# Performance work log

Measured on AMD Instinct MI355X. Metric: run time of the kernel, lower is better.

## Reference

```python
import jax, jax.numpy as jnp
import numpy as np

EPS = 1e-5


def _extract3x3(x, stride=1):
    # channel-major patch extraction: output [B, C*9, Ho, Wo], each channel's 3x3 window contiguous
    B, C, H, W = x.shape
    xp = jnp.pad(x, ((0, 0), (0, 0), (1, 1), (1, 1)))
    Ho = (H + 2 - 3) // stride + 1
    Wo = (W + 2 - 3) // stride + 1
    pats = [xp[:, :, i:i + (Ho - 1) * stride + 1:stride, j:j + (Wo - 1) * stride + 1:stride]
            for i in range(3) for j in range(3)]
    return jnp.stack(pats, axis=2).reshape(B, C * 9, Ho, Wo)


def _amm(patches, centroids, lut, inv_temp):
    # patches: [B, D, H, W] channel-major, D = ncodebooks * subvec_len
    # centroids: [ncb, k, sub], lut: [ncb, k, out_channels]
    B, D, H, W = patches.shape
    ncb, k, sub = centroids.shape
    v = patches.reshape(B, ncb, sub, H * W).transpose(0, 3, 1, 2)  # [B, L, ncb, sub]
    # negative squared distance to each codeword (||v||^2 dropped: constant over k)
    scores = 2.0 * jnp.einsum('blcs,cks->blck', v, centroids) - jnp.sum(centroids * centroids, -1)[None, None]
    attn = jax.nn.softmax(scores * inv_temp, axis=-1)          # soft codeword assignment
    out = jnp.einsum('blck,cko->blo', attn, lut)                # LUT gather/sum over codebooks
    return out.transpose(0, 2, 1).reshape(B, -1, H, W)


def _bn(x, g, b):
    m = x.mean((0, 2, 3), keepdims=True)
    v = x.var((0, 2, 3), keepdims=True)
    return g[None, :, None, None] * (x - m) * jax.lax.rsqrt(v + EPS) + b[None, :, None, None]


def setup_inputs() -> dict:
    key = jax.random.key(0)
    ks = jax.random.split(key, 8)
    B, C, H, W = 32, 1024, 14, 14
    width, out_c, K = 256, 1024, 16
    return {
        'x': jax.random.normal(ks[0], (B, C, H, W), jnp.float32),
        'c1_centroids': jax.random.normal(ks[1], (C // 4, K, 4), jnp.float32),
        'c1_lut': jax.random.normal(ks[2], (C // 4, K, width), jnp.float32) * 0.05,
        'c1_invt': jnp.ones((), jnp.float32),
        'c2_centroids': jax.random.normal(ks[3], (width, K, 9), jnp.float32),
        'c2_lut': jax.random.normal(ks[4], (width, K, width), jnp.float32) * 0.05,
        'c2_invt': jnp.ones((), jnp.float32),
        'c3_centroids': jax.random.normal(ks[5], (width // 4, K, 4), jnp.float32),
        'c3_lut': jax.random.normal(ks[6], (width // 4, K, out_c), jnp.float32) * 0.05,
        'c3_invt': jnp.ones((), jnp.float32),
        'bn1_g': jnp.ones((width,), jnp.float32), 'bn1_b': jnp.zeros((width,), jnp.float32),
        'bn2_g': jnp.ones((width,), jnp.float32), 'bn2_b': jnp.zeros((width,), jnp.float32),
        'bn3_g': jnp.ones((out_c,), jnp.float32), 'bn3_b': jnp.zeros((out_c,), jnp.float32),
    }


def reference(x, c1_centroids, c1_lut, c1_invt, c2_centroids, c2_lut, c2_invt,
              c3_centroids, c3_lut, c3_invt, bn1_g, bn1_b, bn2_g, bn2_b, bn3_g, bn3_b):
    identity = x
    out = _amm(x, c1_centroids, c1_lut, c1_invt)                 # amm_conv1x1, stride 1
    out = jax.nn.relu(_bn(out, bn1_g, bn1_b))
    out = _amm(_extract3x3(out, 1), c2_centroids, c2_lut, c2_invt)  # amm_conv3x3, stride 1, pad 1
    out = jax.nn.relu(_bn(out, bn2_g, bn2_b))
    out = _amm(out, c3_centroids, c3_lut, c3_invt)               # amm_conv1x1
    out = _bn(out, bn3_g, bn3_b)
    return jax.nn.relu(out + identity)
```

## Files before the change

kernel.cpp:

```cpp
#include <hip/hip_runtime.h>
#include <hip/hip_bf16.h>

#define EPSV 1e-5f

typedef unsigned short u16;
typedef __attribute__((ext_vector_type(8))) short short8;
typedef __attribute__((ext_vector_type(4))) float f32x4;
typedef __hip_bfloat16 bf16;

__device__ __forceinline__ unsigned int pack2(float a, float b) {
  bf16 ha = __float2bfloat16(a), hb = __float2bfloat16(b);
  u16 ua, ub;
  __builtin_memcpy(&ua, &ha, 2);
  __builtin_memcpy(&ub, &hb, 2);
  return (unsigned int)ua | ((unsigned int)ub << 16);
}

typedef __attribute__((address_space(1))) const void gvoid_t;
typedef __attribute__((address_space(3))) void lvoid_t;
__device__ __forceinline__ void gload16(const void* g, void* l) {
  __builtin_amdgcn_global_load_lds((gvoid_t*)g, (lvoid_t*)l, 16, 0, 0);
}


__global__ __launch_bounds__(256) void prep_kernel(
    const float* __restrict__ x, const float* __restrict__ cent,
    const float* __restrict__ invt, u16* __restrict__ attn,
    const float* __restrict__ s1, bf16* __restrict__ d1,
    const float* __restrict__ s2, bf16* __restrict__ d2,
    const float* __restrict__ s3, bf16* __restrict__ d3)
{
  __shared__ __align__(16) float sh[4160];
  const int tid = threadIdx.x;
  if (blockIdx.x >= 3584) {
    const int bid = blockIdx.x - 3584;
    const int which = bid >> 8, sub = bid & 255;
    const float* in = (which == 0) ? s1 : (which == 1) ? s2 : s3;
    bf16* out = (which == 0) ? d1 : (which == 1) ? d2 : d3;
    const int K = (which == 2) ? 1024 : 4096;
    const int N = (which == 2) ? 1024 : 256;
    const int kt = K >> 6;
    const int bk = sub & (kt - 1), bn = sub / kt;
    const int k0 = bk * 64, n0 = bn * 64;
    float* t = sh;
    for (int idx = tid; idx < 4096; idx += 256) {
      int r = idx >> 6, c = idx & 63;
      t[r * 65 + c] = in[(size_t)(k0 + r) * N + n0 + c];
    }
    __syncthreads();
    for (int idx = tid; idx < 4096; idx += 256) {
      int r = idx >> 6, c = idx & 63;
      out[(size_t)(n0 + r) * K + k0 + c] = __float2bfloat16(t[c * 65 + r]);
    }
    return;
  }
  float* vs = sh;
  float* cs = sh + 1848;
  const int row = blockIdx.x >> 3, cg = blockIdx.x & 7;
  const int m0 = row * 14;
  const int b = row / 14, y = row - b * 14;
  const float* xb = x + ((size_t)b * 1024 + cg * 128) * 196 + y * 14;
  for (int e = tid; e < 1792; e += 256) {
    int c = e / 14, p = e - c * 14;
    vs[p * 132 + c] = xb[(size_t)c * 196 + p];
  }
  for (int idx = tid; idx < 512; idx += 256) {
    int cb = idx >> 4, kk = idx & 15;
    *(float4*)&cs[cb * 68 + kk * 4] =
        *(const float4*)&cent[(size_t)(cg * 32 + cb) * 64 + kk * 4];
  }
  __syncthreads();
  const float it = invt[0];
  const int cb = tid & 31, pq = tid >> 5;
  const int np = (pq < 6) ? 2 : 1;
  float4 v[2];
  v[0] = *(const float4*)&vs[pq * 132 + cb * 4];
  if (np > 1) v[1] = *(const float4*)&vs[(8 + pq) * 132 + cb * 4];
  float s[2][16];
  #pragma unroll
  for (int k = 0; k < 16; k++) {
    const float4 c = *(const float4*)&cs[cb * 68 + k * 4];
    const float cn = c.x * c.x + c.y * c.y + c.z * c.z + c.w * c.w;
    #pragma unroll
    for (int i = 0; i < 2; i++) if (i < np) {
      float d = v[i].x * c.x + v[i].y * c.y + v[i].z * c.z + v[i].w * c.w;
      s[i][k] = it * (2.f * d - cn);
    }
  }
  #pragma unroll
  for (int i = 0; i < 2; i++) if (i < np) {
    float mx = -3e38f;
    #pragma unroll
    for (int k = 0; k < 16; k++) mx = fmaxf(mx, s[i][k]);
    float sum = 0.f;
    #pragma unroll
    for (int k = 0; k < 16; k++) { float e = __expf(s[i][k] - mx); s[i][k] = e; sum += e; }
    const float r = 1.f / sum;
    uint4 w0, w1;
    w0.x = pack2(s[i][0] * r,  s[i][1] * r);  w0.y = pack2(s[i][2] * r,  s[i][3] * r);
    w0.z = pack2(s[i][4] * r,  s[i][5] * r);  w0.w = pack2(s[i][6] * r,  s[i][7] * r);
    w1.x = pack2(s[i][8] * r,  s[i][9] * r);  w1.y = pack2(s[i][10] * r, s[i][11] * r);
    w1.z = pack2(s[i][12] * r, s[i][13] * r); w1.w = pack2(s[i][14] * r, s[i][15] * r);
    uint4* dst = (uint4*)(attn + (size_t)(m0 + i * 8 + pq) * 4096 + (cg * 32 + cb) * 16);
    dst[0] = w0; dst[1] = w1;
  }
}

__global__ __launch_bounds__(256) void attn2_kernel(const float* __restrict__ out1,
    const float* __restrict__ ss, const float* __restrict__ cent,
    const float* __restrict__ invt, u16* __restrict__ attn)
{
  __shared__ float vs[4 * 16 * 32];
  __shared__ __align__(16) float cs[32 * 196];
  const int tid = threadIdx.x;
  const int rp = blockIdx.x >> 3, cg = blockIdx.x & 7;
  const int b = rp / 7, y0 = (rp % 7) * 2, m0 = rp * 28;
  for (int e = tid; e < 2048; e += 256) {
    int c = e & 31, x1 = (e >> 5) & 15, dyy = e >> 9;
    int yy = y0 + dyy - 1, xx = x1 - 1;
    float v = 0.f;
    int ch = cg * 32 + c;
    if (yy >= 0 && yy < 14 && xx >= 0 && xx < 14) {
      float val = out1[(size_t)((b * 14 + yy) * 14 + xx) * 256 + ch];
      v = fmaxf(val * ss[ch] + ss[256 + ch], 0.f);
    }
    vs[e] = v;
  }
  for (int idx = tid; idx < 1152; idx += 256) {
    int cb = idx / 36, f4i = idx - cb * 36;
    float4 w = *(const float4*)&cent[(size_t)(cg * 32 + cb) * 144 + f4i * 4];
    int j0 = f4i * 4;
    #pragma unroll
    for (int t = 0; t < 4; t++) {
      int j = j0 + t, k = j / 9, jj = j - k * 9;
      cs[cb * 196 + k * 12 + jj] = ((const float*)&w)[t];
    }
  }
  __syncthreads();
  const float it = invt[0];
  const int cb = tid & 31, pq = tid >> 5;
  const int np = (pq < 4) ? 4 : 3;
  float v[4][9];
  #pragma unroll
  for (int i = 0; i < 4; i++) if (i < np) {
    const int p = i * 8 + pq;
    const int r = p / 14, xc = p - r * 14;
    #pragma unroll
    for (int dy = 0; dy < 3; dy++)
      #pragma unroll
      for (int dx = 0; dx < 3; dx++)
        v[i][dy * 3 + dx] = vs[((r + dy) * 16 + xc + dx) * 32 + cb];
  }
  float s[4][16];
  #pragma unroll
  for (int k = 0; k < 16; k++) {
    const float* ck = &cs[cb * 196 + k * 12];
    const float4 ca = *(const float4*)ck;
    const float4 cbv = *(const float4*)(ck + 4);
    const float c8 = ck[8];
    float c9[9] = {ca.x, ca.y, ca.z, ca.w, cbv.x, cbv.y, cbv.z, cbv.w, c8};
    float cn = 0.f;
    #pragma unroll
    for (int j = 0; j < 9; j++) cn = fmaf(c9[j], c9[j], cn);
    #pragma unroll
    for (int i = 0; i < 4; i++) if (i < np) {
      float d = 0.f;
      #pragma unroll
      for (int j = 0; j < 9; j++) d = fmaf(c9[j], v[i][j], d);
      s[i][k] = it * (2.f * d - cn);
    }
  }
  #pragma unroll
  for (int i = 0; i < 4; i++) if (i < np) {
    float mx = -3e38f;
    #pragma unroll
    for (int k = 0; k < 16; k++) mx = fmaxf(mx, s[i][k]);
    float sum = 0.f;
    #pragma unroll
    for (int k = 0; k < 16; k++) { float e = __expf(s[i][k] - mx); s[i][k] = e; sum += e; }
    const float r = 1.f / sum;
    uint4 w0, w1;
    w0.x = pack2(s[i][0] * r,  s[i][1] * r);  w0.y = pack2(s[i][2] * r,  s[i][3] * r);
    w0.z = pack2(s[i][4] * r,  s[i][5] * r);  w0.w = pack2(s[i][6] * r,  s[i][7] * r);
    w1.x = pack2(s[i][8] * r,  s[i][9] * r);  w1.y = pack2(s[i][10] * r, s[i][11] * r);
    w1.z = pack2(s[i][12] * r, s[i][13] * r); w1.w = pack2(s[i][14] * r, s[i][15] * r);
    uint4* dst = (uint4*)(attn + (size_t)(m0 + i * 8 + pq) * 4096 + (cg * 32 + cb) * 16);
    dst[0] = w0; dst[1] = w1;
  }
}

__global__ __launch_bounds__(256) void attn3_kernel(const float* __restrict__ out2,
    const float* __restrict__ ss, const float* __restrict__ cent,
    const float* __restrict__ invt, bf16* __restrict__ attn)
{
  const int t = threadIdx.x;
  const int cb = t & 63, ml = t >> 6;
  const int m0 = blockIdx.x * 16;
  const float it = invt[0];
  float4 cv[16]; float cn[16];
  const float4* cc = (const float4*)(cent + cb * 64);
  #pragma unroll
  for (int k = 0; k < 16; k++) {
    cv[k] = cc[k];
    cn[k] = cv[k].x * cv[k].x + cv[k].y * cv[k].y + cv[k].z * cv[k].z + cv[k].w * cv[k].w;
  }
  const float4 scv = *(const float4*)(ss + cb * 4);
  const float4 shv = *(const float4*)(ss + 256 + cb * 4);
  for (int g = 0; g < 4; g++) {
    const int m = m0 + g * 4 + ml;
    float4 xv = *(const float4*)(out2 + (size_t)m * 256 + cb * 4);
    float4 v;
    v.x = fmaxf(xv.x * scv.x + shv.x, 0.f);
    v.y = fmaxf(xv.y * scv.y + shv.y, 0.f);
    v.z = fmaxf(xv.z * scv.z + shv.z, 0.f);
    v.w = fmaxf(xv.w * scv.w + shv.w, 0.f);
    float s[16], mx = -3e38f;
    #pragma unroll
    for (int k = 0; k < 16; k++) {
      float d = v.x * cv[k].x + v.y * cv[k].y + v.z * cv[k].z + v.w * cv[k].w;
      s[k] = it * (2.f * d - cn[k]);
      mx = fmaxf(mx, s[k]);
    }
    float sum = 0.f;
    #pragma unroll
    for (int k = 0; k < 16; k++) { float e = __expf(s[k] - mx); s[k] = e; sum += e; }
    float r = 1.f / sum;
    #pragma unroll
    for (int k = 0; k < 16; k++)
      attn[(size_t)m * 1024 + cb * 16 + k] = __float2bfloat16(s[k] * r);
  }
}

template<int KDIM, int NT, int KSLICES, int BM, int BK>
__global__ __launch_bounds__(256) void gemm_kernel(const u16* __restrict__ A,
    const u16* __restrict__ Bt, float* __restrict__ C, size_t cstride)
{
  constexpr int NDIM = NT * 128;
  constexpr int KS = KDIM / KSLICES;
  constexpr int MT = 6272 / BM;
  constexpr int FM = BM / 32;
  constexpr int KU = BK / 32;
  constexpr int SLOTS = BK / 8;
  constexpr int RPC = 64 / SLOTS;
  constexpr int ACALLS = BM / (RPC * 4);
  constexpr int BCALLS = 128 / (RPC * 4);
  __shared__ __align__(16) u16 Asm[BM * BK];
  __shared__ __align__(16) u16 Bsm[128 * BK];
  const int tid = threadIdx.x;
  const int nt = blockIdx.x % NT;
  const int mt = (blockIdx.x / NT) % MT;
  const int sl = blockIdx.x / (NT * MT);
  const int kbeg = sl * KS, kend = kbeg + KS;
  const int m0 = mt * BM, n0 = nt * 128;
  const int lane = tid & 63, wid = tid >> 6;
  const int wm = wid >> 1, wn = wid & 1;
  const int lr = lane / SLOTS, sslot = lane % SLOTS;

  f32x4 acc[FM][4];
  #pragma unroll
  for (int i = 0; i < FM; i++)
    #pragma unroll
    for (int j = 0; j < 4; j++) acc[i][j] = (f32x4){0.f, 0.f, 0.f, 0.f};

  const u16* Abase = A + (size_t)m0 * KDIM;
  const u16* Bbase = Bt + (size_t)n0 * KDIM;

  for (int kb = kbeg; kb < kend; kb += BK) {
    #pragma unroll
    for (int c = 0; c < ACALLS; c++) {
      const int r0 = (wid * ACALLS + c) * RPC;
      const int row = r0 + lr;
      const int gs = sslot ^ (row & 7);
      gload16(Abase + (size_t)row * KDIM + kb + gs * 8, &Asm[r0 * BK]);
    }
    #pragma unroll
    for (int c = 0; c < BCALLS; c++) {
      const int r0 = (wid * BCALLS + c) * RPC;
      const int row = r0 + lr;
      const int gs = sslot ^ (row & 7);
      gload16(Bbase + (size_t)row * KDIM + kb + gs * 8, &Bsm[r0 * BK]);
    }
    __syncthreads();
    #pragma unroll
    for (int ks = 0; ks < KU; ks++) {
      short8 a[FM], b[4];
      #pragma unroll
      for (int f = 0; f < FM; f++) {
        const int ra = wm * (BM / 2) + f * 16 + (lane & 15);
        const int ja = (ks * 4 + (lane >> 4)) ^ (ra & 7);
        a[f] = *(const short8*)(Asm + ra * BK + ja * 8);
      }
      #pragma unroll
      for (int f = 0; f < 4; f++) {
        const int rb = wn * 64 + f * 16 + (lane & 15);
        const int jb = (ks * 4 + (lane >> 4)) ^ (rb & 7);
        b[f] = *(const short8*)(Bsm + rb * BK + jb * 8);
      }
      #pragma unroll
      for (int fm = 0; fm < FM; fm++)
        #pragma unroll
        for (int fn = 0; fn < 4; fn++)
          acc[fm][fn] = __builtin_amdgcn_mfma_f32_16x16x32_bf16(a[fm], b[fn], acc[fm][fn], 0, 0, 0);
    }
    __syncthreads();
  }

  float* __restrict__ Cs = C + (size_t)sl * cstride;
  #pragma unroll
  for (int fm = 0; fm < FM; fm++)
    #pragma unroll
    for (int fn = 0; fn < 4; fn++) {
      const int col = n0 + wn * 64 + fn * 16 + (lane & 15);
      const int rbase = m0 + wm * (BM / 2) + fm * 16 + (lane >> 4) * 4;
      #pragma unroll
      for (int r = 0; r < 4; r++)
        Cs[(size_t)(rbase + r) * NDIM + col] = acc[fm][fn][r];
    }
}

template<int CH, int NBLK, int NSUM>
__global__ __launch_bounds__(256) void bnpart_kernel(const float* __restrict__ buf,
    float* __restrict__ sum_out, float* __restrict__ part)
{
  constexpr int PC = CH / 256;
  constexpr int ROWS = 6272 / NBLK;
  constexpr size_t PSTR = 6272ull * CH;
  const int t = threadIdx.x, m0 = blockIdx.x * ROWS;
  float s[PC], s2[PC];
  #pragma unroll
  for (int j = 0; j < PC; j++) { s[j] = 0.f; s2[j] = 0.f; }
  for (int i = 0; i < ROWS; i++) {
    const size_t ro = (size_t)(m0 + i) * CH;
    #pragma unroll
    for (int j = 0; j < PC; j++) {
      float v = buf[ro + t + j * 256];
      #pragma unroll
      for (int n = 1; n < NSUM; n++) v += buf[(size_t)n * PSTR + ro + t + j * 256];
      if (NSUM > 1) sum_out[ro + t + j * 256] = v;
      s[j] += v; s2[j] = fmaf(v, v, s2[j]);
    }
  }
  #pragma unroll
  for (int j = 0; j < PC; j++) {
    part[(size_t)blockIdx.x * (2 * CH) + t + j * 256] = s[j];
    part[(size_t)blockIdx.x * (2 * CH) + CH + t + j * 256] = s2[j];
  }
}

template<int CH, int NBLK>
__global__ __launch_bounds__(256) void bnfin_kernel(const float* __restrict__ part,
    const float* __restrict__ g, const float* __restrict__ bb, float* __restrict__ ss)
{
  __shared__ float red[2][4][64];
  const int t = threadIdx.x;
  const int chl = t & 63, grp = t >> 6;
  const int c = blockIdx.x * 64 + chl;
  float S = 0.f, S2 = 0.f;
  for (int i = grp; i < NBLK; i += 4) {
    S += part[(size_t)i * (2 * CH) + c];
    S2 += part[(size_t)i * (2 * CH) + CH + c];
  }
  red[0][grp][chl] = S; red[1][grp][chl] = S2;
  __syncthreads();
  if (t < 64) {
    float Sf  = red[0][0][t] + red[0][1][t] + red[0][2][t] + red[0][3][t];
    float S2f = red[1][0][t] + red[1][1][t] + red[1][2][t] + red[1][3][t];
    const int ch = blockIdx.x * 64 + t;
    float mean = Sf * (1.f / 6272.f);
    float var = S2f * (1.f / 6272.f) - mean * mean;
    float sc = g[ch] * rsqrtf(var + EPSV);
    ss[ch] = sc;
    ss[CH + ch] = bb[ch] - mean * sc;
  }
}

__global__ __launch_bounds__(256) void tfinal_kernel(const float* __restrict__ out3,
    const float* __restrict__ ss, const float* __restrict__ x, float* __restrict__ out)
{
  __shared__ float t[64 * 199];
  const int b = blockIdx.x >> 4, n0 = (blockIdx.x & 15) * 64;
  for (int idx = threadIdx.x; idx < 196 * 64; idx += 256) {
    int p = idx >> 6, ni = idx & 63;
    float v = out3[(size_t)(b * 196 + p) * 1024 + n0 + ni] * ss[n0 + ni] + ss[1024 + n0 + ni];
    t[ni * 199 + p] = v;
  }
  __syncthreads();
  for (int idx = threadIdx.x; idx < 64 * 196; idx += 256) {
    int ni = idx / 196, p = idx - ni * 196;
    size_t o = (size_t)(b * 1024 + n0 + ni) * 196 + p;
    out[o] = fmaxf(t[ni * 199 + p] + x[o], 0.f);
  }
}


template<int CIN, int OUT, bool APPLY_BN>
__global__ __launch_bounds__(256) void amm1x1_kernel(
    const float* __restrict__ xin, const float* __restrict__ ss,
    const float* __restrict__ cent, const float* __restrict__ lut,
    const float* __restrict__ invt, float* __restrict__ outbuf)
{
  constexpr int NCB = CIN / 4;
  constexpr int NO = OUT / 256;
  __shared__ float vsm[CIN * 14];
  __shared__ __align__(16) float attn_sm[14 * 16];
  const int tid = threadIdx.x;
  const int b = blockIdx.x / 14, y = blockIdx.x % 14;
  const int rowbase = y * 14;
  for (int e = tid; e < CIN * 14; e += 256) {
    int c = e / 14, xc = e - c * 14;
    float v = xin[(b * CIN + c) * 196 + rowbase + xc];
    if (APPLY_BN) v = fmaxf(v * ss[c] + ss[CIN + c], 0.f);
    vsm[e] = v;
  }
  __syncthreads();
  float acc[14 * NO];
  #pragma unroll
  for (int i = 0; i < 14 * NO; i++) acc[i] = 0.f;
  const float it = invt[0];
  const int p_ = tid >> 4, k_ = tid & 15;
  for (int cb = 0; cb < NCB; ++cb) {
    if (tid < 224) {
      const float* cc = cent + (cb * 16 + k_) * 4;
      float s = 0.f;
      #pragma unroll
      for (int si = 0; si < 4; si++) {
        float cv = cc[si];
        float vv = vsm[(cb * 4 + si) * 14 + p_];
        s = fmaf(cv, 2.f * vv - cv, s);
      }
      s *= it;
      float m = s;
      #pragma unroll
      for (int off = 8; off; off >>= 1) m = fmaxf(m, __shfl_xor(m, off, 16));
      float e = __expf(s - m);
      float sum = e;
      #pragma unroll
      for (int off = 8; off; off >>= 1) sum += __shfl_xor(sum, off, 16);
      attn_sm[p_ * 16 + k_] = e / sum;
    }
    __syncthreads();
    float lv[NO][16];
    #pragma unroll
    for (int j = 0; j < NO; j++)
      #pragma unroll
      for (int k = 0; k < 16; k++)
        lv[j][k] = lut[(cb * 16 + k) * OUT + j * 256 + tid];
    const float4* a4 = (const float4*)attn_sm;
    #pragma unroll
    for (int p = 0; p < 14; p++) {
      float4 q0 = a4[p*4+0], q1 = a4[p*4+1], q2 = a4[p*4+2], q3 = a4[p*4+3];
      float av[16] = {q0.x,q0.y,q0.z,q0.w, q1.x,q1.y,q1.z,q1.w,
                      q2.x,q2.y,q2.z,q2.w, q3.x,q3.y,q3.z,q3.w};
      #pragma unroll
      for (int j = 0; j < NO; j++) {
        float s = acc[p * NO + j];
        #pragma unroll
        for (int k = 0; k < 16; k++) s = fmaf(av[k], lv[j][k], s);
        acc[p * NO + j] = s;
      }
    }
    __syncthreads();
  }
  #pragma unroll
  for (int j = 0; j < NO; j++) {
    int o = j * 256 + tid;
    #pragma unroll
    for (int p = 0; p < 14; p++)
      outbuf[(b * OUT + o) * 196 + rowbase + p] = acc[p * NO + j];
  }
}

__global__ __launch_bounds__(256) void amm3x3_kernel(
    const float* __restrict__ xin, const float* __restrict__ ss,
    const float* __restrict__ cent, const float* __restrict__ lut,
    const float* __restrict__ invt, float* __restrict__ outbuf)
{
  __shared__ float vsm[256 * 3 * 16];
  __shared__ __align__(16) float attn_sm[14 * 16];
  const int tid = threadIdx.x;
  const int b = blockIdx.x / 14, y = blockIdx.x % 14;
  for (int e = tid; e < 256 * 3 * 16; e += 256) {
    int c = e / 48, rem = e - c * 48, i = rem >> 4, col = rem & 15;
    int yy = y + i - 1, xx = col - 1;
    float v = 0.f;
    if (yy >= 0 && yy < 14 && xx >= 0 && xx < 14) {
      v = xin[(b * 256 + c) * 196 + yy * 14 + xx];
      v = fmaxf(v * ss[c] + ss[256 + c], 0.f);
    }
    vsm[e] = v;
  }
  __syncthreads();
  float acc[14];
  #pragma unroll
  for (int i = 0; i < 14; i++) acc[i] = 0.f;
  const float it = invt[0];
  const int p_ = tid >> 4, k_ = tid & 15;
  for (int cb = 0; cb < 256; ++cb) {
    if (tid < 224) {
      const float* cc = cent + (cb * 16 + k_) * 9;
      float s = 0.f;
      #pragma unroll
      for (int i = 0; i < 3; i++)
        #pragma unroll
        for (int j = 0; j < 3; j++) {
          float cv = cc[i * 3 + j];
          float vv = vsm[(cb * 3 + i) * 16 + p_ + j];
          s = fmaf(cv, 2.f * vv - cv, s);
        }
      s *= it;
      float m = s;
      #pragma unroll
      for (int off = 8; off; off >>= 1) m = fmaxf(m, __shfl_xor(m, off, 16));
      float e = __expf(s - m);
      float sum = e;
      #pragma unroll
      for (int off = 8; off; off >>= 1) sum += __shfl_xor(sum, off, 16);
      attn_sm[p_ * 16 + k_] = e / sum;
    }
    __syncthreads();
    float lv[16];
    #pragma unroll
    for (int k = 0; k < 16; k++) lv[k] = lut[(cb * 16 + k) * 256 + tid];
    const float4* a4 = (const float4*)attn_sm;
    #pragma unroll
    for (int p = 0; p < 14; p++) {
      float4 q0 = a4[p*4+0], q1 = a4[p*4+1], q2 = a4[p*4+2], q3 = a4[p*4+3];
      float av[16] = {q0.x,q0.y,q0.z,q0.w, q1.x,q1.y,q1.z,q1.w,
                      q2.x,q2.y,q2.z,q2.w, q3.x,q3.y,q3.z,q3.w};
      float s = acc[p];
      #pragma unroll
      for (int k = 0; k < 16; k++) s = fmaf(av[k], lv[k], s);
      acc[p] = s;
    }
    __syncthreads();
  }
  #pragma unroll
  for (int p = 0; p < 14; p++)
    outbuf[(b * 256 + tid) * 196 + y * 14 + p] = acc[p];
}

template<int CH>
__global__ __launch_bounds__(256) void bnstats_kernel(const float* __restrict__ buf,
    const float* __restrict__ g, const float* __restrict__ bb, float* __restrict__ ss)
{
  const int c = blockIdx.x, tid = threadIdx.x;
  float s = 0.f, s2 = 0.f;
  for (int e = tid; e < 32 * 196; e += 256) {
    int bi = e / 196, l = e - bi * 196;
    float v = buf[(bi * CH + c) * 196 + l];
    s += v; s2 = fmaf(v, v, s2);
  }
  #pragma unroll
  for (int off = 32; off; off >>= 1) { s += __shfl_down(s, off); s2 += __shfl_down(s2, off); }
  __shared__ float red[8];
  int w = tid >> 6;
  if ((tid & 63) == 0) { red[w] = s; red[4 + w] = s2; }
  __syncthreads();
  if (tid == 0) {
    float S  = red[0] + red[1] + red[2] + red[3];
    float S2 = red[4] + red[5] + red[6] + red[7];
    float mean = S * (1.f / 6272.f);
    float var  = S2 * (1.f / 6272.f) - mean * mean;
    float sc = g[c] * rsqrtf(var + EPSV);
    ss[c] = sc;
    ss[CH + c] = bb[c] - mean * sc;
  }
}

__global__ __launch_bounds__(256) void final_old_kernel(float* __restrict__ out3,
    const float* __restrict__ ss, const float* __restrict__ x)
{
  const int total = 32 * 1024 * 196;
  for (int idx = blockIdx.x * 256 + threadIdx.x; idx < total; idx += gridDim.x * 256) {
    int c = (idx / 196) & 1023;
    float v = out3[idx] * ss[c] + ss[1024 + c] + x[idx];
    out3[idx] = fmaxf(v, 0.f);
  }
}


extern "C" void kernel_launch(void* const* d_in, const int* in_sizes, int n_in,
                              void* d_out, int out_size, void* d_ws, size_t ws_size,
                              hipStream_t stream) {
  const float* x   = (const float*)d_in[0];
  const float* c1c = (const float*)d_in[1];
  const float* c1l = (const float*)d_in[2];
  const float* c1t = (const float*)d_in[3];
  const float* c2c = (const float*)d_in[4];
  const float* c2l = (const float*)d_in[5];
  const float* c2t = (const float*)d_in[6];
  const float* c3c = (const float*)d_in[7];
  const float* c3l = (const float*)d_in[8];
  const float* c3t = (const float*)d_in[9];
  const float* g1  = (const float*)d_in[10];
  const float* b1  = (const float*)d_in[11];
  const float* g2  = (const float*)d_in[12];
  const float* b2  = (const float*)d_in[13];
  const float* g3  = (const float*)d_in[14];
  const float* b3  = (const float*)d_in[15];

  float* ws = (float*)d_ws;
  const size_t FAST_NEED = 24255488ull * 4ull;

  if (ws_size >= FAST_NEED) {
    u16*   attnB = (u16*)ws;
    float* partC = ws + 12845056;
    float* out1  = partC + 6422528;
    float* out2  = out1 + 1605632;
    bf16*  lutT1 = (bf16*)(out2 + 1605632);
    bf16*  lutT2 = lutT1 + 1048576;
    bf16*  lutT3 = lutT2 + 1048576;
    float* part  = (float*)(lutT3 + 1048576);
    float* ss1   = part + 200704;
    float* ss2   = ss1 + 512;
    float* ss3   = ss2 + 512;
    float* out3  = partC;
    const size_t PART_STRIDE = 1605632;

    prep_kernel<<<4352, 256, 0, stream>>>(x, c1c, c1t, attnB,
                                          c1l, lutT1, c2l, lutT2, c3l, lutT3);

    gemm_kernel<4096, 2, 4, 128, 128><<<392, 256, 0, stream>>>(attnB, (const u16*)lutT1, partC, PART_STRIDE);
    bnpart_kernel<256, 196, 4><<<196, 256, 0, stream>>>(partC, out1, part);
    bnfin_kernel<256, 196><<<4, 256, 0, stream>>>(part, g1, b1, ss1);

    attn2_kernel<<<1792, 256, 0, stream>>>(out1, ss1, c2c, c2t, attnB);
    gemm_kernel<4096, 2, 4, 128, 128><<<392, 256, 0, stream>>>(attnB, (const u16*)lutT2, partC, PART_STRIDE);
    bnpart_kernel<256, 196, 4><<<196, 256, 0, stream>>>(partC, out2, part);
    bnfin_kernel<256, 196><<<4, 256, 0, stream>>>(part, g2, b2, ss2);

    attn3_kernel<<<392, 256, 0, stream>>>(out2, ss2, c3c, c3t, (bf16*)attnB);
    gemm_kernel<1024, 8, 1, 128, 128><<<392, 256, 0, stream>>>(attnB, (const u16*)lutT3, out3, 0);
    bnpart_kernel<1024, 98, 1><<<98, 256, 0, stream>>>(out3, nullptr, part);
    bnfin_kernel<1024, 98><<<16, 256, 0, stream>>>(part, g3, b3, ss3);

    tfinal_kernel<<<512, 256, 0, stream>>>(out3, ss3, x, (float*)d_out);
  } else {
    float* out3 = (float*)d_out;
    float* out1 = ws;
    float* out2 = out1 + 32 * 256 * 196;
    float* ss1  = out2 + 32 * 256 * 196;
    float* ss2  = ss1 + 512;
    float* ss3  = ss2 + 512;

    amm1x1_kernel<1024, 256, false><<<448, 256, 0, stream>>>(x, nullptr, c1c, c1l, c1t, out1);
    bnstats_kernel<256><<<256, 256, 0, stream>>>(out1, g1, b1, ss1);
    amm3x3_kernel<<<448, 256, 0, stream>>>(out1, ss1, c2c, c2l, c2t, out2);
    bnstats_kernel<256><<<256, 256, 0, stream>>>(out2, g2, b2, ss2);
    amm1x1_kernel<256, 1024, true><<<448, 256, 0, stream>>>(out2, ss2, c3c, c3l, c3t, out3);
    bnstats_kernel<1024><<<1024, 256, 0, stream>>>(out3, g3, b3, ss3);
    final_old_kernel<<<2048, 256, 0, stream>>>(out3, ss3, x);
  }
}
```

Before: 324.3 us.

## Retile conv1 softmax prep per batch image and 32-channel group with vectorized loads

The conv1 soft-assignment part of prep_kernel now assigns each block a whole image (196 pixels) for 32 channels (8 codebooks), replacing one spatial row for 128 channels. Input is loaded with float2 reads into a padded LDS tile. Each thread keeps its codebook's centroids and norms in registers and loops over pixels, so the centroid norms are computed once per thread rather than per pixel pair. The block count falls from 3584 to 1024, which cuts launch overhead and repeated centroid loads, but raises LDS use and register pressure and makes the attention writes more strided.

Result: no change. 324.2 us (-0.0%).

```diff
diff --git a/kernel.cpp b/kernel.cpp
--- a/kernel.cpp
+++ b/kernel.cpp
@@ -30,10 +30,10 @@
     const float* __restrict__ s2, bf16* __restrict__ d2,
     const float* __restrict__ s3, bf16* __restrict__ d3)
 {
-  __shared__ __align__(16) float sh[4160];
+  __shared__ __align__(16) float sh[7012];
   const int tid = threadIdx.x;
-  if (blockIdx.x >= 3584) {
-    const int bid = blockIdx.x - 3584;
+  if (blockIdx.x >= 1024) {
+    const int bid = blockIdx.x - 1024;
     const int which = bid >> 8, sub = bid & 255;
     const float* in = (which == 0) ? s1 : (which == 1) ? s2 : s3;
     bf16* out = (which == 0) ? d1 : (which == 1) ? d2 : d3;
@@ -55,53 +55,49 @@
     return;
   }
   float* vs = sh;
-  float* cs = sh + 1848;
-  const int row = blockIdx.x >> 3, cg = blockIdx.x & 7;
-  const int m0 = row * 14;
-  const int b = row / 14, y = row - b * 14;
-  const float* xb = x + ((size_t)b * 1024 + cg * 128) * 196 + y * 14;
-  for (int e = tid; e < 1792; e += 256) {
-    int c = e / 14, p = e - c * 14;
-    vs[p * 132 + c] = xb[(size_t)c * 196 + p];
-  }
-  for (int idx = tid; idx < 512; idx += 256) {
-    int cb = idx >> 4, kk = idx & 15;
+  float* cs = sh + 6468;
+  const int bi = blockIdx.x >> 5, cg = blockIdx.x & 31;
+  const float* xb = x + ((size_t)bi * 1024 + cg * 32) * 196;
+  for (int e = tid; e < 3136; e += 256) {
+    int c = e / 98, p2 = e - c * 98;
+    float2 w = *(const float2*)&xb[(size_t)c * 196 + p2 * 2];
+    vs[(p2 * 2) * 33 + c] = w.x;
+    vs[(p2 * 2 + 1) * 33 + c] = w.y;
+  }
+  if (tid < 128) {
+    int cb = tid >> 4, kk = tid & 15;
     *(float4*)&cs[cb * 68 + kk * 4] =
-        *(const float4*)&cent[(size_t)(cg * 32 + cb) * 64 + kk * 4];
+        *(const float4*)&cent[(size_t)(cg * 8 + cb) * 64 + kk * 4];
   }
   __syncthreads();
   const float it = invt[0];
-  const int cb = tid & 31, pq = tid >> 5;
-  const int np = (pq < 6) ? 2 : 1;
-  float4 v[2];
-  v[0] = *(const float4*)&vs[pq * 132 + cb * 4];
-  if (np > 1) v[1] = *(const float4*)&vs[(8 + pq) * 132 + cb * 4];
-  float s[2][16];
+  const int cbL = tid & 7, pj = tid >> 3;
+  float4 cv[16]; float cn[16];
   #pragma unroll
   for (int k = 0; k < 16; k++) {
-    const float4 c = *(const float4*)&cs[cb * 68 + k * 4];
-    const float cn = c.x * c.x + c.y * c.y + c.z * c.z + c.w * c.w;
-    #pragma unroll
-    for (int i = 0; i < 2; i++) if (i < np) {
-      float d = v[i].x * c.x + v[i].y * c.y + v[i].z * c.z + v[i].w * c.w;
-      s[i][k] = it * (2.f * d - cn);
-    }
-  }
-  #pragma unroll
-  for (int i = 0; i < 2; i++) if (i < np) {
-    float mx = -3e38f;
-    #pragma unroll
-    for (int k = 0; k < 16; k++) mx = fmaxf(mx, s[i][k]);
+    cv[k] = *(const float4*)&cs[cbL * 68 + k * 4];
+    cn[k] = cv[k].x * cv[k].x + cv[k].y * cv[k].y + cv[k].z * cv[k].z + cv[k].w * cv[k].w;
+  }
+  for (int p = pj; p < 196; p += 32) {
+    const float* vp = &vs[p * 33 + cbL * 4];
+    const float v0 = vp[0], v1 = vp[1], v2 = vp[2], v3 = vp[3];
+    float s[16], mx = -3e38f;
+    #pragma unroll
+    for (int k = 0; k < 16; k++) {
+      float d = v0 * cv[k].x + v1 * cv[k].y + v2 * cv[k].z + v3 * cv[k].w;
+      s[k] = it * (2.f * d - cn[k]);
+      mx = fmaxf(mx, s[k]);
+    }
     float sum = 0.f;
     #pragma unroll
-    for (int k = 0; k < 16; k++) { float e = __expf(s[i][k] - mx); s[i][k] = e; sum += e; }
+    for (int k = 0; k < 16; k++) { float e = __expf(s[k] - mx); s[k] = e; sum += e; }
     const float r = 1.f / sum;
     uint4 w0, w1;
-    w0.x = pack2(s[i][0] * r,  s[i][1] * r);  w0.y = pack2(s[i][2] * r,  s[i][3] * r);
-    w0.z = pack2(s[i][4] * r,  s[i][5] * r);  w0.w = pack2(s[i][6] * r,  s[i][7] * r);
-    w1.x = pack2(s[i][8] * r,  s[i][9] * r);  w1.y = pack2(s[i][10] * r, s[i][11] * r);
-    w1.z = pack2(s[i][12] * r, s[i][13] * r); w1.w = pack2(s[i][14] * r, s[i][15] * r);
-    uint4* dst = (uint4*)(attn + (size_t)(m0 + i * 8 + pq) * 4096 + (cg * 32 + cb) * 16);
+    w0.x = pack2(s[0] * r,  s[1] * r);  w0.y = pack2(s[2] * r,  s[3] * r);
+    w0.z = pack2(s[4] * r,  s[5] * r);  w0.w = pack2(s[6] * r,  s[7] * r);
+    w1.x = pack2(s[8] * r,  s[9] * r);  w1.y = pack2(s[10] * r, s[11] * r);
+    w1.z = pack2(s[12] * r, s[13] * r); w1.w = pack2(s[14] * r, s[15] * r);
+    uint4* dst = (uint4*)(attn + (size_t)(bi * 196 + p) * 4096 + (cg * 8 + cbL) * 16);
     dst[0] = w0; dst[1] = w1;
   }
 }
@@ -617,7 +613,7 @@
     float* out3  = partC;
     const size_t PART_STRIDE = 1605632;
 
-    prep_kernel<<<4352, 256, 0, stream>>>(x, c1c, c1t, attnB,
+    prep_kernel<<<1792, 256, 0, stream>>>(x, c1c, c1t, attnB,
                                           c1l, lutT1, c2l, lutT2, c3l, lutT3);
 
     gemm_kernel<4096, 2, 4, 128, 128><<<392, 256, 0, stream>>>(attnB, (const u16*)lutT1, partC, PART_STRIDE);
```
